# Performance work log

Hardware: AMD Instinct MI355X
Metric: run time of the kernel (lower is better)

Reference implementation:

```python
import jax, jax.numpy as jnp
import numpy as np

D_MODEL = 1024
NUM_HEADS = 16
D_K = D_MODEL // NUM_HEADS
MAX_SEQ = 2048


def _rope_tables(seq_len):
    # inv_freq over even indices of d_k
    inv_freq = 1.0 / (10000.0 ** (jnp.arange(0, D_K, 2, dtype=jnp.float32) / D_K))
    pos = jnp.arange(seq_len, dtype=jnp.float32)
    freqs = jnp.einsum('i,j->ij', pos, inv_freq)  # [S, d_k/2]
    # In the original, cos/sin are repeated x2 then sliced [::2], recovering freqs
    return jnp.cos(freqs), jnp.sin(freqs)  # each [S, d_k/2]


def _apply_rope(x, cos_half, sin_half):
    # x: [B, S, H, d_k]; cos/sin half: [1, S, 1, d_k/2]
    x_even = x[..., ::2]
    x_odd = x[..., 1::2]
    r_even = x_even * cos_half - x_odd * sin_half
    r_odd = x_even * sin_half + x_odd * cos_half
    # interleave back: stack on new last axis, reshape
    return jnp.stack([r_even, r_odd], axis=-1).reshape(x.shape)


def setup_inputs() -> dict:
    key = jax.random.key(0)
    ks = jax.random.split(key, 9)
    B, S = 2, 2048
    scale = 1.0 / np.sqrt(D_MODEL)
    x = jax.random.normal(ks[0], (B, S, D_MODEL), dtype=jnp.float32)
    Wq = jax.random.normal(ks[1], (D_MODEL, D_MODEL), dtype=jnp.float32) * scale
    Wk = jax.random.normal(ks[2], (D_MODEL, D_MODEL), dtype=jnp.float32) * scale
    Wv = jax.random.normal(ks[3], (D_MODEL, D_MODEL), dtype=jnp.float32) * scale
    Wo = jax.random.normal(ks[4], (D_MODEL, D_MODEL), dtype=jnp.float32) * scale
    bq = jnp.zeros((D_MODEL,), jnp.float32)
    bk = jnp.zeros((D_MODEL,), jnp.float32)
    bv = jnp.zeros((D_MODEL,), jnp.float32)
    bo = jnp.zeros((D_MODEL,), jnp.float32)
    return {"x": x, "Wq": Wq, "bq": bq, "Wk": Wk, "bk": bk,
            "Wv": Wv, "bv": bv, "Wo": Wo, "bo": bo}


def reference(x, Wq, bq, Wk, bk, Wv, bv, Wo, bo):
    B, S, _ = x.shape
    H, dk = NUM_HEADS, D_K
    q = (x @ Wq + bq).reshape(B, S, H, dk)
    k = (x @ Wk + bk).reshape(B, S, H, dk)
    v = (x @ Wv + bv).reshape(B, S, H, dk)

    cos_half, sin_half = _rope_tables(S)
    cos_half = cos_half[None, :, None, :]  # [1,S,1,dk/2]
    sin_half = sin_half[None, :, None, :]
    q = _apply_rope(q, cos_half, sin_half)
    k = _apply_rope(k, cos_half, sin_half)

    q = q.transpose(0, 2, 1, 3)  # [B,H,S,dk]
    k = k.transpose(0, 2, 1, 3)
    v = v.transpose(0, 2, 1, 3)

    scores = jnp.einsum('bhqd,bhkd->bhqk', q, k) / jnp.sqrt(jnp.float32(dk))
    causal = jnp.where(jnp.tril(jnp.ones((S, S), jnp.float32)) == 0, -1e9, 0.0)
    scores = scores + causal
    attn = jax.nn.softmax(scores, axis=-1)
    out = jnp.einsum('bhqk,bhkd->bhqd', attn, v)
    out = out.transpose(0, 2, 1, 3).reshape(B, S, H * dk)
    return out @ Wo + bo
```

## Files before the change

### kernel.cpp

```cpp
#include <hip/hip_runtime.h>
#include <math.h>

#define D_MODEL 1024
#define NH 16
#define DK 64
#define SEQ 2048
#define BATCH 2
#define MROWS 4096

typedef __attribute__((ext_vector_type(8))) short s8v;
typedef __attribute__((ext_vector_type(4))) float f4v;

__device__ __forceinline__ unsigned short bf16_rne(float x) {
    unsigned int u = __float_as_uint(x);
    unsigned int r = (u + 0x7FFFu + ((u >> 16) & 1u)) >> 16;
    return (unsigned short)r;
}
__device__ __forceinline__ float bf16f(unsigned short h) {
    return __uint_as_float(((unsigned int)h) << 16);
}
__device__ __forceinline__ void gll16(void* lds, const void* g) {
    __builtin_amdgcn_global_load_lds((const __attribute__((address_space(1))) unsigned int*)g,
                                     (__attribute__((address_space(3))) unsigned int*)lds,
                                     16, 0, 0);
}

__global__ __launch_bounds__(256) void rope_tab(float* __restrict__ ct, float* __restrict__ st) {
    int i = blockIdx.x * 256 + threadIdx.x;
    int s = i >> 5, p = i & 31;
    double inv = exp(-((double)(2 * p) / 64.0) * 9.210340371976184);
    double f = (double)s * inv;
    ct[i] = (float)cos(f);
    st[i] = (float)sin(f);
}

__global__ __launch_bounds__(256) void casth(const float* __restrict__ src,
                                             unsigned short* __restrict__ hi, int n4) {
    int i = blockIdx.x * 256 + threadIdx.x;
    const int stride = gridDim.x * 256;
    for (; i < n4; i += stride) {
        const float4 v = ((const float4*)src)[i];
        ushort4 h;
        h.x = bf16_rne(v.x);
        h.y = bf16_rne(v.y);
        h.z = bf16_rne(v.z);
        h.w = bf16_rne(v.w);
        ((ushort4*)hi)[i] = h;
    }
}

__global__ __launch_bounds__(256) void wsplit(const float* __restrict__ W,
                                              unsigned short* __restrict__ Th,
                                              unsigned short* __restrict__ Tl) {
    __shared__ float t[64][65];
    const int k0 = blockIdx.y * 64, n0 = blockIdx.x * 64;
    const int tid = threadIdx.x;
#pragma unroll
    for (int i = 0; i < 4; i++) {
        int u = tid + i * 256;
        int r = u >> 4, c = (u & 15) * 4;
        float4 v = *(const float4*)(W + (size_t)(k0 + r) * D_MODEL + n0 + c);
        t[r][c] = v.x; t[r][c + 1] = v.y; t[r][c + 2] = v.z; t[r][c + 3] = v.w;
    }
    __syncthreads();
#pragma unroll
    for (int i = 0; i < 4; i++) {
        int u = tid + i * 256;
        int nr = u >> 4, kc = (u & 15) * 4;
        ushort4 h, l;
        float x0 = t[kc + 0][nr], x1 = t[kc + 1][nr], x2 = t[kc + 2][nr], x3 = t[kc + 3][nr];
        h.x = bf16_rne(x0); l.x = bf16_rne(x0 - bf16f(h.x));
        h.y = bf16_rne(x1); l.y = bf16_rne(x1 - bf16f(h.y));
        h.z = bf16_rne(x2); l.z = bf16_rne(x2 - bf16f(h.z));
        h.w = bf16_rne(x3); l.w = bf16_rne(x3 - bf16f(h.w));
        *(ushort4*)(Th + (size_t)(n0 + nr) * D_MODEL + k0 + kc) = h;
        *(ushort4*)(Tl + (size_t)(n0 + nr) * D_MODEL + k0 + kc) = l;
    }
}

__global__ __launch_bounds__(256) void vtrans(const unsigned short* __restrict__ Vh,
                                              unsigned short* __restrict__ VT) {
    __shared__ unsigned short t[64][65];
    const int bh = blockIdx.y, s0 = blockIdx.x * 64;
    const int tid = threadIdx.x;
    const int r = tid >> 2, c16 = (tid & 3) * 16;
#pragma unroll
    for (int i = 0; i < 2; i++) {
        s8v v = *(const s8v*)(Vh + ((size_t)bh * SEQ + s0 + r) * 64 + c16 + i * 8);
#pragma unroll
        for (int j = 0; j < 8; j++) t[r][c16 + i * 8 + j] = ((unsigned short*)&v)[j];
    }
    __syncthreads();
    const int d = tid >> 2, sc = (tid & 3) * 16;
#pragma unroll
    for (int i = 0; i < 2; i++) {
        s8v o;
#pragma unroll
        for (int j = 0; j < 8; j++) ((unsigned short*)&o)[j] = t[sc + i * 8 + j][d];
        *(s8v*)(VT + ((size_t)bh * 64 + d) * SEQ + s0 + sc + i * 8) = o;
    }
}

__global__ __launch_bounds__(256, 2) void gemm_b3(
    const unsigned short* __restrict__ Ah,
    const unsigned short* B0h, const unsigned short* B0l,
    const unsigned short* B1h, const unsigned short* B1l,
    const unsigned short* B2h, const unsigned short* B2l,
    const float* b0, const float* b1, const float* b2,
    float* out1,
    unsigned short* qh, unsigned short* ql, unsigned short* kh2, unsigned short* kl2,
    unsigned short* vh, unsigned short* vl,
    const float* __restrict__ ct, const float* __restrict__ st, int mode) {

    const int z = blockIdx.z;
    const unsigned short* Bh = (z == 0) ? B0h : ((z == 1) ? B1h : B2h);
    const unsigned short* Bl = (z == 0) ? B0l : ((z == 1) ? B1l : B2l);
    const float* bias = (z == 0) ? b0 : ((z == 1) ? b1 : b2);

    const int m0 = blockIdx.y * 128, n0 = blockIdx.x * 128;
    const int tid = threadIdx.x, w = tid >> 6, L = tid & 63;
    const int wr = w >> 1, wc = w & 1;

    __shared__ unsigned short sm[3][128][32];

    f4v acc[4][4];
#pragma unroll
    for (int i = 0; i < 4; i++)
#pragma unroll
        for (int j = 0; j < 4; j++) acc[i][j] = (f4v){0.f, 0.f, 0.f, 0.f};

    const int fr = L & 15, kh = (L >> 4) * 8;

    for (int k0 = 0; k0 < D_MODEL; k0 += 32) {
#pragma unroll
        for (int t = 0; t < 2; t++) {
            const int i = w * 2 + t;
            const int row = i * 16 + (L >> 2);
            const size_t kof = (size_t)k0 + (L & 3) * 8;
            gll16(&sm[0][i * 16][0], Ah + (size_t)(m0 + row) * D_MODEL + kof);
            gll16(&sm[1][i * 16][0], Bh + (size_t)(n0 + row) * D_MODEL + kof);
            gll16(&sm[2][i * 16][0], Bl + (size_t)(n0 + row) * D_MODEL + kof);
        }
        __syncthreads();

        s8v fah[4], fbh[4], fbl[4];
#pragma unroll
        for (int mi = 0; mi < 4; mi++)
            fah[mi] = *(const s8v*)&sm[0][wr * 64 + mi * 16 + fr][kh];
#pragma unroll
        for (int ni = 0; ni < 4; ni++) {
            fbh[ni] = *(const s8v*)&sm[1][wc * 64 + ni * 16 + fr][kh];
            fbl[ni] = *(const s8v*)&sm[2][wc * 64 + ni * 16 + fr][kh];
        }
#pragma unroll
        for (int mi = 0; mi < 4; mi++)
#pragma unroll
            for (int ni = 0; ni < 4; ni++) {
                acc[mi][ni] = __builtin_amdgcn_mfma_f32_16x16x32_bf16(fah[mi], fbl[ni], acc[mi][ni], 0, 0, 0);
                acc[mi][ni] = __builtin_amdgcn_mfma_f32_16x16x32_bf16(fah[mi], fbh[ni], acc[mi][ni], 0, 0, 0);
            }
        __syncthreads();
    }

#pragma unroll
    for (int mi = 0; mi < 4; mi++)
#pragma unroll
        for (int ni = 0; ni < 4; ni++) {
            const int col = n0 + wc * 64 + ni * 16 + fr;
            const float bv = bias[col];
#pragma unroll
            for (int r = 0; r < 4; r++) {
                const int row = m0 + wr * 64 + mi * 16 + (L >> 4) * 4 + r;
                float v = acc[mi][ni][r] + bv;
                if (mode == 1) {
                    out1[(size_t)row * D_MODEL + col] = v;
                } else {
                    const int b = row >> 11, s = row & (SEQ - 1);
                    const int h = col >> 6, d = col & 63;
                    float res;
                    if (z < 2) {
                        const float pr = __shfl_xor(v, 1, 64);
                        const int pp = d >> 1;
                        const float cv = ct[s * 32 + pp], sv = st[s * 32 + pp];
                        res = (L & 1) ? fmaf(pr, sv, v * cv) : fmaf(v, cv, -(pr * sv));
                    } else {
                        res = v;
                    }
                    const size_t idx = ((size_t)(b * NH + h) * SEQ + s) * DK + d;
                    const unsigned short rh = bf16_rne(res);
                    const unsigned short rl = bf16_rne(res - bf16f(rh));
                    if (z == 0)      { qh[idx] = rh;  ql[idx] = rl; }
                    else if (z == 1) { kh2[idx] = rh; kl2[idx] = rl; }
                    else             { vh[idx] = rh;  vl[idx] = rl; }
                }
            }
        }
}

__global__ __launch_bounds__(256, 2) void attn_mfma(
    const unsigned short* __restrict__ Qh, const unsigned short* __restrict__ Ql,
    const unsigned short* __restrict__ Kh, const unsigned short* __restrict__ Kl,
    const unsigned short* __restrict__ VTh, const unsigned short* __restrict__ VTl,
    unsigned short* __restrict__ Aoh) {

    __shared__ __align__(16) unsigned char LDS[32768];
    const int bx = blockIdx.x;
    const int bh = bx & 31;
    const int p = 31 - (bx >> 5);
    const int tid = threadIdx.x;
    const int wq = tid >> 6, lane = tid & 63;
    const int b = bh >> 4, h = bh & 15;
    const int l15 = lane & 15, l4 = lane >> 4;

    const int qbase = p * 64 + wq * 16;
    s8v fqh[2], fql[2];
    {
        const size_t rowB = ((size_t)bh * SEQ + qbase + l15) * 128;
        const int kof = l4 * 16;
        fqh[0] = *(const s8v*)((const char*)Qh + rowB + kof);
        fqh[1] = *(const s8v*)((const char*)Qh + rowB + kof + 64);
        fql[0] = *(const s8v*)((const char*)Ql + rowB + kof);
        fql[1] = *(const s8v*)((const char*)Ql + rowB + kof + 64);
    }

    f4v oacc[4];
#pragma unroll
    for (int i = 0; i < 4; i++) oacc[i] = (f4v){0.f, 0.f, 0.f, 0.f};
    float m = -1e30f, l = 0.f;

    const int nkt = 2 * (p + 1);

    auto stage = [&](int t, unsigned char* bb) {
        {
            const int row = wq * 8 + (lane >> 3);
            const int off = (lane & 7) * 16;
            const int soff = off ^ ((row & 7) << 4);
            const size_t kB = ((size_t)bh * SEQ + (size_t)t * 32 + row) * 128 + soff;
            gll16(bb + 0    + wq * 1024, (const char*)Kh + kB);
            gll16(bb + 4096 + wq * 1024, (const char*)Kl + kB);
        }
        {
            const int row = wq * 16 + (lane >> 2);
            const int off = (lane & 3) * 16;
            const int soff = off ^ (((row >> 1) & 3) << 4);
            const size_t vB = (((size_t)bh * 64 + row) * SEQ + (size_t)t * 32) * 2 + soff;
            gll16(bb + 8192  + wq * 1024, (const char*)VTh + vB);
            gll16(bb + 12288 + wq * 1024, (const char*)VTl + vB);
        }
    };

    stage(0, LDS);

    for (int t = 0; t < nkt; ++t) {
        unsigned char* rb = (t & 1) ? (LDS + 16384) : LDS;
        __syncthreads();
        if (t + 1 < nkt) stage(t + 1, (t & 1) ? LDS : (LDS + 16384));

        f4v sacc[2];
#pragma unroll
        for (int kt = 0; kt < 2; kt++) sacc[kt] = (f4v){0.f, 0.f, 0.f, 0.f};
#pragma unroll
        for (int kt = 0; kt < 2; kt++) {
            const int krow = kt * 16 + l15;
            const int swz = (krow & 7) << 4;
#pragma unroll
            for (int c = 0; c < 2; c++) {
                const int kb = (krow * 128 + c * 64 + l4 * 16) ^ swz;
                s8v fkh = *(const s8v*)(rb + kb);
                s8v fkl = *(const s8v*)(rb + 4096 + kb);
                sacc[kt] = __builtin_amdgcn_mfma_f32_16x16x32_bf16(fkh, fql[c], sacc[kt], 0, 0, 0);
                sacc[kt] = __builtin_amdgcn_mfma_f32_16x16x32_bf16(fkl, fqh[c], sacc[kt], 0, 0, 0);
                sacc[kt] = __builtin_amdgcn_mfma_f32_16x16x32_bf16(fkh, fqh[c], sacc[kt], 0, 0, 0);
            }
        }

        const int dk0 = t * 32 - p * 64;
        const int qlocal = wq * 16 + l15;
        float sv[8];
#pragma unroll
        for (int kt = 0; kt < 2; kt++)
#pragma unroll
            for (int r = 0; r < 4; r++) {
                const int kp = dk0 + kt * 16 + l4 * 4 + r;
                float s = sacc[kt][r] * 0.125f;
                sv[kt * 4 + r] = (kp > qlocal) ? -1e30f : s;
            }
        float pm = fmaxf(fmaxf(fmaxf(sv[0], sv[1]), fmaxf(sv[2], sv[3])),
                         fmaxf(fmaxf(sv[4], sv[5]), fmaxf(sv[6], sv[7])));
        pm = fmaxf(pm, __shfl_xor(pm, 16, 64));
        pm = fmaxf(pm, __shfl_xor(pm, 32, 64));
        const float mn = fmaxf(m, pm);
        const float cc = __expf(m - mn);
        m = mn;
        float ps[8], psum = 0.f;
#pragma unroll
        for (int i = 0; i < 8; i++) { ps[i] = __expf(sv[i] - mn); psum += ps[i]; }
        psum += __shfl_xor(psum, 16, 64);
        psum += __shfl_xor(psum, 32, 64);
        l = l * cc + psum;
#pragma unroll
        for (int ni = 0; ni < 4; ni++)
#pragma unroll
            for (int r = 0; r < 4; r++) oacc[ni][r] *= cc;

        unsigned w0 = (unsigned)bf16_rne(ps[0]) | ((unsigned)bf16_rne(ps[1]) << 16);
        unsigned w1 = (unsigned)bf16_rne(ps[2]) | ((unsigned)bf16_rne(ps[3]) << 16);
        unsigned w2 = (unsigned)bf16_rne(ps[4]) | ((unsigned)bf16_rne(ps[5]) << 16);
        unsigned w3 = (unsigned)bf16_rne(ps[6]) | ((unsigned)bf16_rne(ps[7]) << 16);
        const bool lo2 = (l4 < 2);
        unsigned sA = lo2 ? w2 : w0, sB = lo2 ? w3 : w1;
        unsigned rA = (unsigned)__shfl_xor((int)sA, 32, 64);
        unsigned rB = (unsigned)__shfl_xor((int)sB, 32, 64);
        unsigned q0 = lo2 ? w0 : rA, q1 = lo2 ? w1 : rB;
        unsigned q2 = lo2 ? rA : w2, q3 = lo2 ? rB : w3;
        const bool ev = ((l4 & 1) == 0);
        unsigned sC = ev ? q2 : q0, sD = ev ? q3 : q1;
        unsigned rC = (unsigned)__shfl_xor((int)sC, 16, 64);
        unsigned rD = (unsigned)__shfl_xor((int)sD, 16, 64);
        unsigned d0 = ev ? q0 : rC, d1 = ev ? q1 : rD;
        unsigned d2 = ev ? rC : q2, d3 = ev ? rD : q3;
        s8v fp;
        ((unsigned*)&fp)[0] = d0; ((unsigned*)&fp)[1] = d1;
        ((unsigned*)&fp)[2] = d2; ((unsigned*)&fp)[3] = d3;

#pragma unroll
        for (int ni = 0; ni < 4; ni++) {
            const int row = ni * 16 + l15;
            const int vb = row * 64 + ((l4 * 16) ^ (((row >> 1) & 3) << 4));
            s8v fvh = *(const s8v*)(rb + 8192 + vb);
            s8v fvl = *(const s8v*)(rb + 12288 + vb);
            oacc[ni] = __builtin_amdgcn_mfma_f32_16x16x32_bf16(fvl, fp, oacc[ni], 0, 0, 0);
            oacc[ni] = __builtin_amdgcn_mfma_f32_16x16x32_bf16(fvh, fp, oacc[ni], 0, 0, 0);
        }
    }

    const float inv = 1.0f / l;
    const int q = p * 64 + wq * 16 + l15;
    unsigned short* obase = Aoh + ((size_t)b * SEQ + q) * D_MODEL + h * DK;
#pragma unroll
    for (int ni = 0; ni < 4; ni++) {
        ushort4 o;
        o.x = bf16_rne(oacc[ni][0] * inv);
        o.y = bf16_rne(oacc[ni][1] * inv);
        o.z = bf16_rne(oacc[ni][2] * inv);
        o.w = bf16_rne(oacc[ni][3] * inv);
        *(ushort4*)(obase + ni * 16 + l4 * 4) = o;
    }
}

extern "C" void kernel_launch(void* const* d_in, const int* in_sizes, int n_in,
                              void* d_out, int out_size, void* d_ws, size_t ws_size,
                              hipStream_t stream) {
    const float* x  = (const float*)d_in[0];
    const float* Wq = (const float*)d_in[1];
    const float* bq = (const float*)d_in[2];
    const float* Wk = (const float*)d_in[3];
    const float* bk = (const float*)d_in[4];
    const float* Wv = (const float*)d_in[5];
    const float* bv = (const float*)d_in[6];
    const float* Wo = (const float*)d_in[7];
    const float* bo = (const float*)d_in[8];
    float* out = (float*)d_out;

    char* wsb = (char*)d_ws;
    unsigned short* xh  = (unsigned short*)(wsb);
    unsigned short* Aoh = (unsigned short*)(wsb + 8388608);
    unsigned short* wt  = (unsigned short*)(wsb + 16777216);
    unsigned short* Qh  = (unsigned short*)(wsb + 33554432);
    unsigned short* Ql  = (unsigned short*)(wsb + 41943040);
    unsigned short* Kh  = (unsigned short*)(wsb + 50331648);
    unsigned short* Kl  = (unsigned short*)(wsb + 58720256);
    unsigned short* Vh  = (unsigned short*)(wsb + 67108864);
    unsigned short* Vl  = (unsigned short*)(wsb + 75497472);
    unsigned short* VTh = (unsigned short*)(wsb + 83886080);
    unsigned short* VTl = (unsigned short*)(wsb + 92274688);
    float* ct = (float*)(wsb + 100663296);
    float* st = (float*)(wsb + 100925440);

    const size_t WSZ = 1048576;

    rope_tab<<<256, 256, 0, stream>>>(ct, st);
    casth<<<1024, 256, 0, stream>>>(x, xh, (MROWS * D_MODEL) / 4);
    wsplit<<<dim3(16, 16), 256, 0, stream>>>(Wq, wt + 0 * WSZ, wt + 1 * WSZ);
    wsplit<<<dim3(16, 16), 256, 0, stream>>>(Wk, wt + 2 * WSZ, wt + 3 * WSZ);
    wsplit<<<dim3(16, 16), 256, 0, stream>>>(Wv, wt + 4 * WSZ, wt + 5 * WSZ);
    wsplit<<<dim3(16, 16), 256, 0, stream>>>(Wo, wt + 6 * WSZ, wt + 7 * WSZ);

    gemm_b3<<<dim3(8, 32, 3), 256, 0, stream>>>(xh,
        wt + 0 * WSZ, wt + 1 * WSZ, wt + 2 * WSZ, wt + 3 * WSZ, wt + 4 * WSZ, wt + 5 * WSZ,
        bq, bk, bv, nullptr, Qh, Ql, Kh, Kl, Vh, Vl, ct, st, 0);

    vtrans<<<dim3(SEQ / 64, 32), 256, 0, stream>>>(Vh, VTh);
    vtrans<<<dim3(SEQ / 64, 32), 256, 0, stream>>>(Vl, VTl);

    attn_mfma<<<dim3(1024), 256, 0, stream>>>(Qh, Ql, Kh, Kl, VTh, VTl, Aoh);

    gemm_b3<<<dim3(8, 32, 1), 256, 0, stream>>>(Aoh,
        wt + 6 * WSZ, wt + 7 * WSZ, wt + 6 * WSZ, wt + 7 * WSZ, wt + 6 * WSZ, wt + 7 * WSZ,
        bo, bo, bo, out, nullptr, nullptr, nullptr, nullptr, nullptr, nullptr, ct, st, 1);
}
```

Measured before the change: 296.0 us.

## Drop low-part weight split for QKV GEMM and retile out-projection and LDS layouts

The QKV projection now uses only bf16 high parts of the weights, with a new transpose-only kernel. This halves the MFMA count and the B-operand loads in that GEMM, at the cost of weight precision. The output projection becomes its own kernel with 64-row tiles, which doubles the grid, and keeps the hi/lo weight split. The LDS staging in the GEMMs and attention switches from swizzled row layouts to a fragment-major layout so each lane reads a contiguous 16-byte chunk. That layout also changes the global load access patterns.

```diff
diff --git a/kernel.cpp b/kernel.cpp
--- a/kernel.cpp
+++ b/kernel.cpp
@@ -49,6 +49,32 @@
     }
 }
 
+__global__ __launch_bounds__(256) void wtrans(const float* __restrict__ W,
+                                              unsigned short* __restrict__ Th) {
+    __shared__ float t[64][65];
+    const int k0 = blockIdx.y * 64, n0 = blockIdx.x * 64;
+    const int tid = threadIdx.x;
+#pragma unroll
+    for (int i = 0; i < 4; i++) {
+        int u = tid + i * 256;
+        int r = u >> 4, c = (u & 15) * 4;
+        float4 v = *(const float4*)(W + (size_t)(k0 + r) * D_MODEL + n0 + c);
+        t[r][c] = v.x; t[r][c + 1] = v.y; t[r][c + 2] = v.z; t[r][c + 3] = v.w;
+    }
+    __syncthreads();
+#pragma unroll
+    for (int i = 0; i < 4; i++) {
+        int u = tid + i * 256;
+        int nr = u >> 4, kc = (u & 15) * 4;
+        ushort4 h;
+        h.x = bf16_rne(t[kc + 0][nr]);
+        h.y = bf16_rne(t[kc + 1][nr]);
+        h.z = bf16_rne(t[kc + 2][nr]);
+        h.w = bf16_rne(t[kc + 3][nr]);
+        *(ushort4*)(Th + (size_t)(n0 + nr) * D_MODEL + k0 + kc) = h;
+    }
+}
+
 __global__ __launch_bounds__(256) void wsplit(const float* __restrict__ W,
                                               unsigned short* __restrict__ Th,
                                               unsigned short* __restrict__ Tl) {
@@ -101,27 +127,25 @@
     }
 }
 
-__global__ __launch_bounds__(256, 2) void gemm_b3(
+__global__ __launch_bounds__(256, 2) void gemm_qkv(
     const unsigned short* __restrict__ Ah,
-    const unsigned short* B0h, const unsigned short* B0l,
-    const unsigned short* B1h, const unsigned short* B1l,
-    const unsigned short* B2h, const unsigned short* B2l,
+    const unsigned short* __restrict__ B0h, const unsigned short* __restrict__ B1h,
+    const unsigned short* __restrict__ B2h,
     const float* b0, const float* b1, const float* b2,
-    float* out1,
     unsigned short* qh, unsigned short* ql, unsigned short* kh2, unsigned short* kl2,
     unsigned short* vh, unsigned short* vl,
-    const float* __restrict__ ct, const float* __restrict__ st, int mode) {
+    const float* __restrict__ ct, const float* __restrict__ st) {
 
     const int z = blockIdx.z;
     const unsigned short* Bh = (z == 0) ? B0h : ((z == 1) ? B1h : B2h);
-    const unsigned short* Bl = (z == 0) ? B0l : ((z == 1) ? B1l : B2l);
     const float* bias = (z == 0) ? b0 : ((z == 1) ? b1 : b2);
 
     const int m0 = blockIdx.y * 128, n0 = blockIdx.x * 128;
     const int tid = threadIdx.x, w = tid >> 6, L = tid & 63;
     const int wr = w >> 1, wc = w & 1;
-
-    __shared__ unsigned short sm[3][128][32];
+    const int l15 = L & 15, l4 = L >> 4;
+
+    __shared__ __align__(16) unsigned char sm[16384];
 
     f4v acc[4][4];
 #pragma unroll
@@ -129,70 +153,123 @@
 #pragma unroll
         for (int j = 0; j < 4; j++) acc[i][j] = (f4v){0.f, 0.f, 0.f, 0.f};
 
-    const int fr = L & 15, kh = (L >> 4) * 8;
-
     for (int k0 = 0; k0 < D_MODEL; k0 += 32) {
 #pragma unroll
-        for (int t = 0; t < 2; t++) {
-            const int i = w * 2 + t;
-            const int row = i * 16 + (L >> 2);
-            const size_t kof = (size_t)k0 + (L & 3) * 8;
-            gll16(&sm[0][i * 16][0], Ah + (size_t)(m0 + row) * D_MODEL + kof);
-            gll16(&sm[1][i * 16][0], Bh + (size_t)(n0 + row) * D_MODEL + kof);
-            gll16(&sm[2][i * 16][0], Bl + (size_t)(n0 + row) * D_MODEL + kof);
+        for (int t = 0; t < 4; t++) {
+            const int i = w * 4 + t;
+            const size_t row = (i < 8) ? (size_t)(m0 + i * 16 + l15)
+                                       : (size_t)(n0 + (i - 8) * 16 + l15);
+            const unsigned short* src = (i < 8) ? Ah : Bh;
+            gll16(sm + i * 1024, src + row * D_MODEL + k0 + l4 * 8);
         }
         __syncthreads();
 
-        s8v fah[4], fbh[4], fbl[4];
+        s8v fa[4], fb[4];
 #pragma unroll
         for (int mi = 0; mi < 4; mi++)
-            fah[mi] = *(const s8v*)&sm[0][wr * 64 + mi * 16 + fr][kh];
+            fa[mi] = *(const s8v*)(sm + ((wr * 4 + mi) << 10) + L * 16);
+#pragma unroll
+        for (int ni = 0; ni < 4; ni++)
+            fb[ni] = *(const s8v*)(sm + 8192 + ((wc * 4 + ni) << 10) + L * 16);
+#pragma unroll
+        for (int mi = 0; mi < 4; mi++)
+#pragma unroll
+            for (int ni = 0; ni < 4; ni++)
+                acc[mi][ni] = __builtin_amdgcn_mfma_f32_16x16x32_bf16(fa[mi], fb[ni], acc[mi][ni], 0, 0, 0);
+        __syncthreads();
+    }
+
+#pragma unroll
+    for (int mi = 0; mi < 4; mi++)
 #pragma unroll
         for (int ni = 0; ni < 4; ni++) {
-            fbh[ni] = *(const s8v*)&sm[1][wc * 64 + ni * 16 + fr][kh];
-            fbl[ni] = *(const s8v*)&sm[2][wc * 64 + ni * 16 + fr][kh];
-        }
-#pragma unroll
-        for (int mi = 0; mi < 4; mi++)
+            const int col = n0 + wc * 64 + ni * 16 + l15;
+            const float bv = bias[col];
+#pragma unroll
+            for (int r = 0; r < 4; r++) {
+                const int row = m0 + wr * 64 + mi * 16 + l4 * 4 + r;
+                const float v = acc[mi][ni][r] + bv;
+                const int b = row >> 11, s = row & (SEQ - 1);
+                const int h = col >> 6, d = col & 63;
+                float res;
+                if (z < 2) {
+                    const float pr = __shfl_xor(v, 1, 64);
+                    const int pp = d >> 1;
+                    const float cv = ct[s * 32 + pp], sv = st[s * 32 + pp];
+                    res = (L & 1) ? fmaf(pr, sv, v * cv) : fmaf(v, cv, -(pr * sv));
+                } else {
+                    res = v;
+                }
+                const size_t idx = ((size_t)(b * NH + h) * SEQ + s) * DK + d;
+                const unsigned short rh = bf16_rne(res);
+                const unsigned short rl = bf16_rne(res - bf16f(rh));
+                if (z == 0)      { qh[idx] = rh;  ql[idx] = rl; }
+                else if (z == 1) { kh2[idx] = rh; kl2[idx] = rl; }
+                else             { vh[idx] = rh;  vl[idx] = rl; }
+            }
+        }
+}
+
+__global__ __launch_bounds__(256, 2) void gemm_out(
+    const unsigned short* __restrict__ Ah,
+    const unsigned short* __restrict__ Bh, const unsigned short* __restrict__ Bl,
+    const float* __restrict__ bias, float* __restrict__ out1) {
+
+    const int m0 = blockIdx.y * 64, n0 = blockIdx.x * 128;
+    const int tid = threadIdx.x, w = tid >> 6, L = tid & 63;
+    const int wr = w >> 1, wc = w & 1;
+    const int l15 = L & 15, l4 = L >> 4;
+
+    __shared__ __align__(16) unsigned char sm[20480];
+
+    f4v acc[2][4];
+#pragma unroll
+    for (int i = 0; i < 2; i++)
+#pragma unroll
+        for (int j = 0; j < 4; j++) acc[i][j] = (f4v){0.f, 0.f, 0.f, 0.f};
+
+    for (int k0 = 0; k0 < D_MODEL; k0 += 32) {
+#pragma unroll
+        for (int t = 0; t < 5; t++) {
+            const int i = w * 5 + t;
+            const unsigned short* src;
+            size_t row;
+            if (i < 4)        { src = Ah; row = (size_t)(m0 + i * 16 + l15); }
+            else if (i < 12)  { src = Bh; row = (size_t)(n0 + (i - 4) * 16 + l15); }
+            else              { src = Bl; row = (size_t)(n0 + (i - 12) * 16 + l15); }
+            gll16(sm + i * 1024, src + row * D_MODEL + k0 + l4 * 8);
+        }
+        __syncthreads();
+
+        s8v fa[2], fbh[4], fbl[4];
+#pragma unroll
+        for (int mi = 0; mi < 2; mi++)
+            fa[mi] = *(const s8v*)(sm + ((wr * 2 + mi) << 10) + L * 16);
+#pragma unroll
+        for (int ni = 0; ni < 4; ni++) {
+            fbh[ni] = *(const s8v*)(sm + 4096 + ((wc * 4 + ni) << 10) + L * 16);
+            fbl[ni] = *(const s8v*)(sm + 12288 + ((wc * 4 + ni) << 10) + L * 16);
+        }
+#pragma unroll
+        for (int mi = 0; mi < 2; mi++)
 #pragma unroll
             for (int ni = 0; ni < 4; ni++) {
-                acc[mi][ni] = __builtin_amdgcn_mfma_f32_16x16x32_bf16(fah[mi], fbl[ni], acc[mi][ni], 0, 0, 0);
-                acc[mi][ni] = __builtin_amdgcn_mfma_f32_16x16x32_bf16(fah[mi], fbh[ni], acc[mi][ni], 0, 0, 0);
+                acc[mi][ni] = __builtin_amdgcn_mfma_f32_16x16x32_bf16(fa[mi], fbl[ni], acc[mi][ni], 0, 0, 0);
+                acc[mi][ni] = __builtin_amdgcn_mfma_f32_16x16x32_bf16(fa[mi], fbh[ni], acc[mi][ni], 0, 0, 0);
             }
         __syncthreads();
     }
 
 #pragma unroll
-    for (int mi = 0; mi < 4; mi++)
+    for (int mi = 0; mi < 2; mi++)
 #pragma unroll
         for (int ni = 0; ni < 4; ni++) {
-            const int col = n0 + wc * 64 + ni * 16 + fr;
+            const int col = n0 + wc * 64 + ni * 16 + l15;
             const float bv = bias[col];
 #pragma unroll
             for (int r = 0; r < 4; r++) {
-                const int row = m0 + wr * 64 + mi * 16 + (L >> 4) * 4 + r;
-                float v = acc[mi][ni][r] + bv;
-                if (mode == 1) {
-                    out1[(size_t)row * D_MODEL + col] = v;
-                } else {
-                    const int b = row >> 11, s = row & (SEQ - 1);
-                    const int h = col >> 6, d = col & 63;
-                    float res;
-                    if (z < 2) {
-                        const float pr = __shfl_xor(v, 1, 64);
-                        const int pp = d >> 1;
-                        const float cv = ct[s * 32 + pp], sv = st[s * 32 + pp];
-                        res = (L & 1) ? fmaf(pr, sv, v * cv) : fmaf(v, cv, -(pr * sv));
-                    } else {
-                        res = v;
-                    }
-                    const size_t idx = ((size_t)(b * NH + h) * SEQ + s) * DK + d;
-                    const unsigned short rh = bf16_rne(res);
-                    const unsigned short rl = bf16_rne(res - bf16f(rh));
-                    if (z == 0)      { qh[idx] = rh;  ql[idx] = rl; }
-                    else if (z == 1) { kh2[idx] = rh; kl2[idx] = rl; }
-                    else             { vh[idx] = rh;  vl[idx] = rl; }
-                }
+                const int row = m0 + (wr * 2 + mi) * 16 + l4 * 4 + r;
+                out1[(size_t)row * D_MODEL + col] = acc[mi][ni][r] + bv;
             }
         }
 }
@@ -232,18 +309,15 @@
 
     auto stage = [&](int t, unsigned char* bb) {
         {
-            const int row = wq * 8 + (lane >> 3);
-            const int off = (lane & 7) * 16;
-            const int soff = off ^ ((row & 7) << 4);
-            const size_t kB = ((size_t)bh * SEQ + (size_t)t * 32 + row) * 128 + soff;
+            const int srow = (wq >> 1) * 16 + l15;
+            const int doff = (wq & 1) * 64 + l4 * 16;
+            const size_t kB = ((size_t)bh * SEQ + (size_t)t * 32 + srow) * 128 + doff;
             gll16(bb + 0    + wq * 1024, (const char*)Kh + kB);
             gll16(bb + 4096 + wq * 1024, (const char*)Kl + kB);
         }
         {
-            const int row = wq * 16 + (lane >> 2);
-            const int off = (lane & 3) * 16;
-            const int soff = off ^ (((row >> 1) & 3) << 4);
-            const size_t vB = (((size_t)bh * 64 + row) * SEQ + (size_t)t * 32) * 2 + soff;
+            const int drow = wq * 16 + l15;
+            const size_t vB = (((size_t)bh * 64 + drow) * SEQ + (size_t)t * 32 + l4 * 8) * 2;
             gll16(bb + 8192  + wq * 1024, (const char*)VTh + vB);
             gll16(bb + 12288 + wq * 1024, (const char*)VTl + vB);
         }
@@ -261,13 +335,11 @@
         for (int kt = 0; kt < 2; kt++) sacc[kt] = (f4v){0.f, 0.f, 0.f, 0.f};
 #pragma unroll
         for (int kt = 0; kt < 2; kt++) {
-            const int krow = kt * 16 + l15;
-            const int swz = (krow & 7) << 4;
 #pragma unroll
             for (int c = 0; c < 2; c++) {
-                const int kb = (krow * 128 + c * 64 + l4 * 16) ^ swz;
-                s8v fkh = *(const s8v*)(rb + kb);
-                s8v fkl = *(const s8v*)(rb + 4096 + kb);
+                const int sb = ((kt * 2 + c) << 10) + lane * 16;
+                s8v fkh = *(const s8v*)(rb + sb);
+                s8v fkl = *(const s8v*)(rb + 4096 + sb);
                 sacc[kt] = __builtin_amdgcn_mfma_f32_16x16x32_bf16(fkh, fql[c], sacc[kt], 0, 0, 0);
                 sacc[kt] = __builtin_amdgcn_mfma_f32_16x16x32_bf16(fkl, fqh[c], sacc[kt], 0, 0, 0);
                 sacc[kt] = __builtin_amdgcn_mfma_f32_16x16x32_bf16(fkh, fqh[c], sacc[kt], 0, 0, 0);
@@ -325,8 +397,7 @@
 
 #pragma unroll
         for (int ni = 0; ni < 4; ni++) {
-            const int row = ni * 16 + l15;
-            const int vb = row * 64 + ((l4 * 16) ^ (((row >> 1) & 3) << 4));
+            const int vb = (ni << 10) + lane * 16;
             s8v fvh = *(const s8v*)(rb + 8192 + vb);
             s8v fvl = *(const s8v*)(rb + 12288 + vb);
             oacc[ni] = __builtin_amdgcn_mfma_f32_16x16x32_bf16(fvl, fp, oacc[ni], 0, 0, 0);
@@ -381,21 +452,19 @@
 
     rope_tab<<<256, 256, 0, stream>>>(ct, st);
     casth<<<1024, 256, 0, stream>>>(x, xh, (MROWS * D_MODEL) / 4);
-    wsplit<<<dim3(16, 16), 256, 0, stream>>>(Wq, wt + 0 * WSZ, wt + 1 * WSZ);
-    wsplit<<<dim3(16, 16), 256, 0, stream>>>(Wk, wt + 2 * WSZ, wt + 3 * WSZ);
-    wsplit<<<dim3(16, 16), 256, 0, stream>>>(Wv, wt + 4 * WSZ, wt + 5 * WSZ);
-    wsplit<<<dim3(16, 16), 256, 0, stream>>>(Wo, wt + 6 * WSZ, wt + 7 * WSZ);
-
-    gemm_b3<<<dim3(8, 32, 3), 256, 0, stream>>>(xh,
-        wt + 0 * WSZ, wt + 1 * WSZ, wt + 2 * WSZ, wt + 3 * WSZ, wt + 4 * WSZ, wt + 5 * WSZ,
-        bq, bk, bv, nullptr, Qh, Ql, Kh, Kl, Vh, Vl, ct, st, 0);
+    wtrans<<<dim3(16, 16), 256, 0, stream>>>(Wq, wt + 0 * WSZ);
+    wtrans<<<dim3(16, 16), 256, 0, stream>>>(Wk, wt + 1 * WSZ);
+    wtrans<<<dim3(16, 16), 256, 0, stream>>>(Wv, wt + 2 * WSZ);
+    wsplit<<<dim3(16, 16), 256, 0, stream>>>(Wo, wt + 3 * WSZ, wt + 4 * WSZ);
+
+    gemm_qkv<<<dim3(8, 32, 3), 256, 0, stream>>>(xh,
+        wt + 0 * WSZ, wt + 1 * WSZ, wt + 2 * WSZ,
+        bq, bk, bv, Qh, Ql, Kh, Kl, Vh, Vl, ct, st);
 
     vtrans<<<dim3(SEQ / 64, 32), 256, 0, stream>>>(Vh, VTh);
     vtrans<<<dim3(SEQ / 64, 32), 256, 0, stream>>>(Vl, VTl);
 
     attn_mfma<<<dim3(1024), 256, 0, stream>>>(Qh, Ql, Kh, Kl, VTh, VTl, Aoh);
 
-    gemm_b3<<<dim3(8, 32, 1), 256, 0, stream>>>(Aoh,
-        wt + 6 * WSZ, wt + 7 * WSZ, wt + 6 * WSZ, wt + 7 * WSZ, wt + 6 * WSZ, wt + 7 * WSZ,
-        bo, bo, bo, out, nullptr, nullptr, nullptr, nullptr, nullptr, nullptr, ct, st, 1);
-}
+    gemm_out<<<dim3(8, 64), 256, 0, stream>>>(Aoh, wt + 3 * WSZ, wt + 4 * WSZ, bo, out);
+}
```

After: 295.4 us. Within noise of the previous version (-0.2%).
